# Performance work log

Hardware: AMD Instinct MI355X
Metric: run time of the kernel (lower is better)

## Reference

```python
import jax, jax.numpy as jnp
from jax import lax
import numpy as np

T, B, I, H = 512, 64, 512, 512


def setup_inputs() -> dict:
    key = jax.random.key(0)
    k0, k1, k2, k3, k4 = jax.random.split(key, 5)
    s = 1.0 / np.sqrt(H)  # PyTorch LSTM init range
    x = jax.random.normal(k0, (T, B, I), dtype=jnp.float32)
    W_ih = jax.random.uniform(k1, (4 * H, I), jnp.float32, -s, s)
    W_hh = jax.random.uniform(k2, (4 * H, H), jnp.float32, -s, s)
    b_ih = jax.random.uniform(k3, (4 * H,), jnp.float32, -s, s)
    b_hh = jax.random.uniform(k4, (4 * H,), jnp.float32, -s, s)
    return {"x": x, "W_ih": W_ih, "W_hh": W_hh, "b_ih": b_ih, "b_hh": b_hh}


def reference(x, W_ih, W_hh, b_ih, b_hh):
    # x: [T, B, I] (seq-first, like nn.LSTM with batch_first=False)
    Bv = x.shape[1]
    Hv = W_hh.shape[1]
    # Precompute input projections for all timesteps: [T, B, 4H]
    x_proj = jnp.einsum('tbi,gi->tbg', x, W_ih) + b_ih + b_hh

    def step(carry, xp):
        h, c = carry
        gates = xp + h @ W_hh.T  # [B, 4H]
        i, f, g, o = jnp.split(gates, 4, axis=-1)  # PyTorch gate order i,f,g,o
        i = jax.nn.sigmoid(i)
        f = jax.nn.sigmoid(f)
        g = jnp.tanh(g)
        o = jax.nn.sigmoid(o)
        c = f * c + i * g
        h = o * jnp.tanh(c)
        return (h, c), h

    h0 = jnp.zeros((Bv, Hv), dtype=x.dtype)
    c0 = jnp.zeros((Bv, Hv), dtype=x.dtype)
    _, ys = lax.scan(step, (h0, c0), x_proj)
    return ys  # [T, B, H]
```

## Files before the change

### kernel.cpp

```cpp
#include <hip/hip_runtime.h>


#define T_STEPS 512
#define BATCH   64
#define HID     512
#define NB      64
#define CNT_STRIDE 16

typedef short bf16x8 __attribute__((ext_vector_type(8)));
typedef float f32x4  __attribute__((ext_vector_type(4)));

struct U16B { unsigned long long x, y; };

__device__ __forceinline__ unsigned short f2bf(float f) {
    unsigned int u = __builtin_bit_cast(unsigned int, f);
    u += 0x7FFFu + ((u >> 16) & 1u);
    return (unsigned short)(u >> 16);
}
__device__ __forceinline__ unsigned int pack2(float lo, float hi) {
    return (unsigned int)f2bf(lo) | ((unsigned int)f2bf(hi) << 16);
}
__device__ __forceinline__ uint4 cvt8(const float* __restrict__ p) {
    float4 f0 = *(const float4*)p;
    float4 f1 = *(const float4*)(p + 4);
    uint4 r;
    r.x = pack2(f0.x, f0.y);
    r.y = pack2(f0.z, f0.w);
    r.z = pack2(f1.x, f1.y);
    r.w = pack2(f1.z, f1.w);
    return r;
}
__device__ __forceinline__ void store_cg16(void* p, uint4 v) {
    unsigned long long* q = (unsigned long long*)p;
    U16B u = __builtin_bit_cast(U16B, v);
    __hip_atomic_store(q,     u.x, __ATOMIC_RELAXED, __HIP_MEMORY_SCOPE_AGENT);
    __hip_atomic_store(q + 1, u.y, __ATOMIC_RELAXED, __HIP_MEMORY_SCOPE_AGENT);
}
__device__ __forceinline__ float sigmoidf_(float x) {
    return 1.0f / (1.0f + __expf(-x));
}
__device__ __forceinline__ float tanhf_(float x) {
    x = fminf(fmaxf(x, -15.f), 15.f);
    float e = __expf(2.0f * x);
    return (e - 1.0f) / (e + 1.0f);
}

extern "C" __global__ void __launch_bounds__(256, 1)
lstm_fused(const float* __restrict__ x,
           const float* __restrict__ W_ih,
           const float* __restrict__ W_hh,
           const float* __restrict__ b_ih,
           const float* __restrict__ b_hh,
           float* __restrict__ out,
           unsigned int* __restrict__ cnt,
           unsigned short* __restrict__ hbuf)
{
    __shared__ uint4 sB[2][2][16][64];
    __shared__ __align__(16) unsigned short sH[4][16][8];
    __shared__ __align__(16) float          sHf[4][16][8];

    const int blk  = blockIdx.x;
    const int tid  = threadIdx.x;
    const int w    = tid >> 6;
    const int lane = tid & 63;
    const int l15  = lane & 15;
    const int quad = lane >> 4;
    const int hc0  = blk * 8;

    for (int u = tid; u < 2 * 16 * 64; u += 256) {
        int nt   = u >> 10;
        int kk   = (u >> 6) & 15;
        int ln   = u & 63;
        int c    = (ln & 15) + (nt << 4);
        int grow = ((c >> 3) << 9) + hc0 + (c & 7);
        int k0   = kk * 32 + ((ln >> 4) << 3);
        sB[0][nt][kk][ln] = cvt8(W_ih + grow * 512 + k0);
        sB[1][nt][kk][ln] = cvt8(W_hh + grow * 512 + k0);
    }

    float bias0, bias1;
    {
        int c0 = l15,      g0 = ((c0 >> 3) << 9) + hc0 + (c0 & 7);
        int c1 = l15 + 16, g1 = ((c1 >> 3) << 9) + hc0 + (c1 & 7);
        bias0 = b_ih[g0] + b_hh[g0];
        bias1 = b_ih[g1] + b_hh[g1];
    }
    __syncthreads();

    float cst[4] = {0.f, 0.f, 0.f, 0.f};
    const int aoff = (((w << 4) + l15) * 512) + (quad << 3);
    char* const hb_base = (char*)hbuf;
    const int   hread_off = (quad << 10) + (((w << 4) + l15) << 4);
    long long budget = 300000LL;

    for (int t = 0; t < T_STEPS; ++t) {
        f32x4 acc0 = {0.f, 0.f, 0.f, 0.f};
        f32x4 acc1 = {0.f, 0.f, 0.f, 0.f};

        const float* xt = x + (size_t)t * (BATCH * 512) + aoff;
#pragma unroll
        for (int kk = 0; kk < 16; ++kk) {
            bf16x8 a  = __builtin_bit_cast(bf16x8, cvt8(xt + kk * 32));
            bf16x8 b0 = __builtin_bit_cast(bf16x8, sB[0][0][kk][lane]);
            bf16x8 b1 = __builtin_bit_cast(bf16x8, sB[0][1][kk][lane]);
            acc0 = __builtin_amdgcn_mfma_f32_16x16x32_bf16(a, b0, acc0, 0, 0, 0);
            acc1 = __builtin_amdgcn_mfma_f32_16x16x32_bf16(a, b1, acc1, 0, 0, 0);
        }

        if (t > 0) {
            if (tid == 0) {
                const unsigned int* cp = cnt + (size_t)(t - 1) * CNT_STRIDE;
                while (budget > 0) {
                    unsigned int v = __hip_atomic_load(cp, __ATOMIC_RELAXED,
                                                       __HIP_MEMORY_SCOPE_AGENT);
                    if (v >= NB) break;
                    __builtin_amdgcn_s_sleep(1);
                    --budget;
                }
            }
            __syncthreads();

            const char* hp = hb_base + (((t - 1) & 1) << 16) + hread_off;
            U16B ha[16];
#pragma unroll
            for (int kk = 0; kk < 16; ++kk) {
                const unsigned long long* q =
                    (const unsigned long long*)(hp + (kk << 12));
                ha[kk].x = __hip_atomic_load(q,     __ATOMIC_RELAXED,
                                             __HIP_MEMORY_SCOPE_AGENT);
                ha[kk].y = __hip_atomic_load(q + 1, __ATOMIC_RELAXED,
                                             __HIP_MEMORY_SCOPE_AGENT);
            }
#pragma unroll
            for (int kk = 0; kk < 16; ++kk) {
                bf16x8 a  = __builtin_bit_cast(bf16x8, ha[kk]);
                bf16x8 b0 = __builtin_bit_cast(bf16x8, sB[1][0][kk][lane]);
                bf16x8 b1 = __builtin_bit_cast(bf16x8, sB[1][1][kk][lane]);
                acc0 = __builtin_amdgcn_mfma_f32_16x16x32_bf16(a, b0, acc0, 0, 0, 0);
                acc1 = __builtin_amdgcn_mfma_f32_16x16x32_bf16(a, b1, acc1, 0, 0, 0);
            }
        }

        float gi[4], gf[4], gg[4], go[4];
#pragma unroll
        for (int r = 0; r < 4; ++r) {
            float a0 = acc0[r] + bias0;
            float a1 = acc1[r] + bias1;
            float p0 = __shfl_xor(a0, 8, 64);
            float p1 = __shfl_xor(a1, 8, 64);
            gi[r] = a0; gg[r] = a1; gf[r] = p0; go[r] = p1;
        }
        if (l15 < 8) {
#pragma unroll
            for (int r = 0; r < 4; ++r) {
                float iv = sigmoidf_(gi[r]);
                float fv = sigmoidf_(gf[r]);
                float gv = tanhf_(gg[r]);
                float ov = sigmoidf_(go[r]);
                cst[r] = fv * cst[r] + iv * gv;
                float hv = ov * tanhf_(cst[r]);
                sH [w][(quad << 2) + r][l15] = f2bf(hv);
                sHf[w][(quad << 2) + r][l15] = hv;
            }
        }
        asm volatile("s_waitcnt lgkmcnt(0)" ::: "memory");
        if (lane < 16) {
            uint4 v = *(const uint4*)&sH[w][lane][0];
            char* dst = hb_base + ((t & 1) << 16) + (blk << 10)
                        + (((w << 4) + lane) << 4);
            store_cg16(dst, v);
        }
        asm volatile("s_waitcnt vmcnt(0)" ::: "memory");
        __syncthreads();
        if (tid == 0) {
            (void)__hip_atomic_fetch_add(cnt + (size_t)t * CNT_STRIDE, 1u,
                                         __ATOMIC_RELAXED, __HIP_MEMORY_SCOPE_AGENT);
        }

        if (lane < 32) {
            int row  = lane & 15;
            int half = lane >> 4;
            uint4 v = *(const uint4*)&sHf[w][row][half << 2];
            float* op = out + (size_t)t * (BATCH * HID)
                        + (size_t)((w << 4) + row) * HID + hc0 + (half << 2);
            *(uint4*)op = v;
        }
    }
}

extern "C" void kernel_launch(void* const* d_in, const int* in_sizes, int n_in,
                              void* d_out, int out_size, void* d_ws, size_t ws_size,
                              hipStream_t stream) {
    const float* x    = (const float*)d_in[0];
    const float* W_ih = (const float*)d_in[1];
    const float* W_hh = (const float*)d_in[2];
    const float* b_ih = (const float*)d_in[3];
    const float* b_hh = (const float*)d_in[4];
    float* out = (float*)d_out;

    unsigned int*   cnt = (unsigned int*)d_ws;
    const size_t    cnt_bytes = (size_t)T_STEPS * CNT_STRIDE * sizeof(unsigned int);
    unsigned short* hbuf = (unsigned short*)((char*)d_ws + cnt_bytes);

    (void)hipMemsetAsync(cnt, 0, cnt_bytes, stream);

    hipLaunchKernelGGL(lstm_fused, dim3(NB), dim3(256), 0, stream,
                       x, W_ih, W_hh, b_ih, b_hh, out, cnt, hbuf);
}
```

Before: 3.948 ms.

## Replace global step counter barrier with per-wave flag polling across blocks

Result: slower. 4.030 ms (+2.1%).

```diff
diff --git a/kernel.cpp b/kernel.cpp
--- a/kernel.cpp
+++ b/kernel.cpp
@@ -5,7 +5,6 @@
 #define BATCH   64
 #define HID     512
 #define NB      64
-#define CNT_STRIDE 16
 
 typedef short bf16x8 __attribute__((ext_vector_type(8)));
 typedef float f32x4  __attribute__((ext_vector_type(4)));
@@ -52,7 +51,7 @@
            const float* __restrict__ b_ih,
            const float* __restrict__ b_hh,
            float* __restrict__ out,
-           unsigned int* __restrict__ cnt,
+           unsigned int* __restrict__ flags,
            unsigned short* __restrict__ hbuf)
 {
     __shared__ uint4 sB[2][2][16][64];
@@ -91,9 +90,17 @@
     const int aoff = (((w << 4) + l15) * 512) + (quad << 3);
     char* const hb_base = (char*)hbuf;
     const int   hread_off = (quad << 10) + (((w << 4) + l15) << 4);
-    long long budget = 300000LL;
+    unsigned int* const       my_flag = flags + (w << 6) + blk;
+    const unsigned int* const poll_p  = flags + (w << 6) + lane;
+    long long budget = 400000LL;
 
     for (int t = 0; t < T_STEPS; ++t) {
+        unsigned int early = 0u;
+        if (t > 0)
+            early = __hip_atomic_load(poll_p, __ATOMIC_RELAXED,
+                                      __HIP_MEMORY_SCOPE_AGENT);
+        __builtin_amdgcn_sched_barrier(0);
+
         f32x4 acc0 = {0.f, 0.f, 0.f, 0.f};
         f32x4 acc1 = {0.f, 0.f, 0.f, 0.f};
 
@@ -108,17 +115,15 @@
         }
 
         if (t > 0) {
-            if (tid == 0) {
-                const unsigned int* cp = cnt + (size_t)(t - 1) * CNT_STRIDE;
+            const unsigned int tgt = (unsigned int)t;
+            if (!__all(early >= tgt)) {
                 while (budget > 0) {
-                    unsigned int v = __hip_atomic_load(cp, __ATOMIC_RELAXED,
+                    unsigned int v = __hip_atomic_load(poll_p, __ATOMIC_RELAXED,
                                                        __HIP_MEMORY_SCOPE_AGENT);
-                    if (v >= NB) break;
-                    __builtin_amdgcn_s_sleep(1);
+                    if (__all(v >= tgt)) break;
                     --budget;
                 }
             }
-            __syncthreads();
 
             const char* hp = hb_base + (((t - 1) & 1) << 16) + hread_off;
             U16B ha[16];
@@ -171,10 +176,9 @@
             store_cg16(dst, v);
         }
         asm volatile("s_waitcnt vmcnt(0)" ::: "memory");
-        __syncthreads();
-        if (tid == 0) {
-            (void)__hip_atomic_fetch_add(cnt + (size_t)t * CNT_STRIDE, 1u,
-                                         __ATOMIC_RELAXED, __HIP_MEMORY_SCOPE_AGENT);
+        if (lane == 0) {
+            __hip_atomic_store(my_flag, (unsigned int)(t + 1),
+                               __ATOMIC_RELAXED, __HIP_MEMORY_SCOPE_AGENT);
         }
 
         if (lane < 32) {
@@ -198,12 +202,12 @@
     const float* b_hh = (const float*)d_in[4];
     float* out = (float*)d_out;
 
-    unsigned int*   cnt = (unsigned int*)d_ws;
-    const size_t    cnt_bytes = (size_t)T_STEPS * CNT_STRIDE * sizeof(unsigned int);
-    unsigned short* hbuf = (unsigned short*)((char*)d_ws + cnt_bytes);
-
-    (void)hipMemsetAsync(cnt, 0, cnt_bytes, stream);
+    unsigned int*   flags = (unsigned int*)d_ws;
+    const size_t    flag_bytes = 4 * NB * sizeof(unsigned int);
+    unsigned short* hbuf = (unsigned short*)((char*)d_ws + 1024);
+
+    (void)hipMemsetAsync(flags, 0, flag_bytes, stream);
 
     hipLaunchKernelGGL(lstm_fused, dim3(NB), dim3(256), 0, stream,
-                       x, W_ih, W_hh, b_ih, b_hh, out, cnt, hbuf);
-}
+                       x, W_ih, W_hh, b_ih, b_hh, out, flags, hbuf);
+}
```

## Replace counter barrier with per-element step tags in hidden-state buffer

Applied to the files above, without the earlier changes.

New measurement: 4.037 ms. 1.02x slower.

```diff
diff --git a/kernel.cpp b/kernel.cpp
--- a/kernel.cpp
+++ b/kernel.cpp
@@ -5,7 +5,6 @@
 #define BATCH   64
 #define HID     512
 #define NB      64
-#define CNT_STRIDE 16
 
 typedef short bf16x8 __attribute__((ext_vector_type(8)));
 typedef float f32x4  __attribute__((ext_vector_type(4)));
@@ -52,12 +51,11 @@
            const float* __restrict__ b_ih,
            const float* __restrict__ b_hh,
            float* __restrict__ out,
-           unsigned int* __restrict__ cnt,
-           unsigned short* __restrict__ hbuf)
+           unsigned int* __restrict__ hbuf)
 {
     __shared__ uint4 sB[2][2][16][64];
-    __shared__ __align__(16) unsigned short sH[4][16][8];
-    __shared__ __align__(16) float          sHf[4][16][8];
+    __shared__ __align__(16) unsigned int sHt[4][16][8];
+    __shared__ __align__(16) float        sHf[4][16][8];
 
     const int blk  = blockIdx.x;
     const int tid  = threadIdx.x;
@@ -89,9 +87,9 @@
 
     float cst[4] = {0.f, 0.f, 0.f, 0.f};
     const int aoff = (((w << 4) + l15) * 512) + (quad << 3);
-    char* const hb_base = (char*)hbuf;
-    const int   hread_off = (quad << 10) + (((w << 4) + l15) << 4);
-    long long budget = 300000LL;
+    char* const hb_base  = (char*)hbuf;
+    const int   hread_off = (quad << 11) + (((w << 4) + l15) << 5);
+    long long budget = 2000000LL;
 
     for (int t = 0; t < T_STEPS; ++t) {
         f32x4 acc0 = {0.f, 0.f, 0.f, 0.f};
@@ -108,32 +106,42 @@
         }
 
         if (t > 0) {
-            if (tid == 0) {
-                const unsigned int* cp = cnt + (size_t)(t - 1) * CNT_STRIDE;
-                while (budget > 0) {
-                    unsigned int v = __hip_atomic_load(cp, __ATOMIC_RELAXED,
-                                                       __HIP_MEMORY_SCOPE_AGENT);
-                    if (v >= NB) break;
-                    __builtin_amdgcn_s_sleep(1);
-                    --budget;
+            const char* hp = hb_base + (((t - 1) & 1) << 17) + hread_off;
+            const unsigned int tgt = (unsigned int)t;
+            unsigned long long hw[64];
+            for (;;) {
+#pragma unroll
+                for (int kk = 0; kk < 16; ++kk) {
+                    const unsigned long long* q =
+                        (const unsigned long long*)(hp + (kk << 13));
+#pragma unroll
+                    for (int j = 0; j < 4; ++j)
+                        hw[kk * 4 + j] = __hip_atomic_load(q + j, __ATOMIC_RELAXED,
+                                                           __HIP_MEMORY_SCOPE_AGENT);
                 }
+                unsigned int m = 0;
+#pragma unroll
+                for (int i = 0; i < 64; ++i)
+                    m |= ((unsigned int)hw[i] ^ tgt) & 0xffffu;
+                if (__all(m == 0)) break;
+                if (--budget < 0) break;
             }
-            __syncthreads();
-
-            const char* hp = hb_base + (((t - 1) & 1) << 16) + hread_off;
-            U16B ha[16];
 #pragma unroll
             for (int kk = 0; kk < 16; ++kk) {
-                const unsigned long long* q =
-                    (const unsigned long long*)(hp + (kk << 12));
-                ha[kk].x = __hip_atomic_load(q,     __ATOMIC_RELAXED,
-                                             __HIP_MEMORY_SCOPE_AGENT);
-                ha[kk].y = __hip_atomic_load(q + 1, __ATOMIC_RELAXED,
-                                             __HIP_MEMORY_SCOPE_AGENT);
-            }
-#pragma unroll
-            for (int kk = 0; kk < 16; ++kk) {
-                bf16x8 a  = __builtin_bit_cast(bf16x8, ha[kk]);
+                unsigned int w0 = (unsigned int)(hw[4 * kk + 0]);
+                unsigned int w1 = (unsigned int)(hw[4 * kk + 0] >> 32);
+                unsigned int w2 = (unsigned int)(hw[4 * kk + 1]);
+                unsigned int w3 = (unsigned int)(hw[4 * kk + 1] >> 32);
+                unsigned int w4 = (unsigned int)(hw[4 * kk + 2]);
+                unsigned int w5 = (unsigned int)(hw[4 * kk + 2] >> 32);
+                unsigned int w6 = (unsigned int)(hw[4 * kk + 3]);
+                unsigned int w7 = (unsigned int)(hw[4 * kk + 3] >> 32);
+                uint4 u;
+                u.x = (w0 >> 16) | (w1 & 0xffff0000u);
+                u.y = (w2 >> 16) | (w3 & 0xffff0000u);
+                u.z = (w4 >> 16) | (w5 & 0xffff0000u);
+                u.w = (w6 >> 16) | (w7 & 0xffff0000u);
+                bf16x8 a  = __builtin_bit_cast(bf16x8, u);
                 bf16x8 b0 = __builtin_bit_cast(bf16x8, sB[1][0][kk][lane]);
                 bf16x8 b1 = __builtin_bit_cast(bf16x8, sB[1][1][kk][lane]);
                 acc0 = __builtin_amdgcn_mfma_f32_16x16x32_bf16(a, b0, acc0, 0, 0, 0);
@@ -150,6 +158,7 @@
             float p1 = __shfl_xor(a1, 8, 64);
             gi[r] = a0; gg[r] = a1; gf[r] = p0; go[r] = p1;
         }
+        const unsigned int tagv = (unsigned int)(t + 1);
         if (l15 < 8) {
 #pragma unroll
             for (int r = 0; r < 4; ++r) {
@@ -159,22 +168,19 @@
                 float ov = sigmoidf_(go[r]);
                 cst[r] = fv * cst[r] + iv * gv;
                 float hv = ov * tanhf_(cst[r]);
-                sH [w][(quad << 2) + r][l15] = f2bf(hv);
+                sHt[w][(quad << 2) + r][l15] =
+                    ((unsigned int)f2bf(hv) << 16) | tagv;
                 sHf[w][(quad << 2) + r][l15] = hv;
             }
         }
         asm volatile("s_waitcnt lgkmcnt(0)" ::: "memory");
-        if (lane < 16) {
-            uint4 v = *(const uint4*)&sH[w][lane][0];
-            char* dst = hb_base + ((t & 1) << 16) + (blk << 10)
-                        + (((w << 4) + lane) << 4);
+        if (lane < 32) {
+            int row  = lane >> 1;
+            int half = lane & 1;
+            uint4 v = *(const uint4*)&sHt[w][row][half << 2];
+            char* dst = hb_base + ((t & 1) << 17) + (blk << 11)
+                        + (((w << 4) + row) << 5) + (half << 4);
             store_cg16(dst, v);
-        }
-        asm volatile("s_waitcnt vmcnt(0)" ::: "memory");
-        __syncthreads();
-        if (tid == 0) {
-            (void)__hip_atomic_fetch_add(cnt + (size_t)t * CNT_STRIDE, 1u,
-                                         __ATOMIC_RELAXED, __HIP_MEMORY_SCOPE_AGENT);
         }
 
         if (lane < 32) {
@@ -198,12 +204,9 @@
     const float* b_hh = (const float*)d_in[4];
     float* out = (float*)d_out;
 
-    unsigned int*   cnt = (unsigned int*)d_ws;
-    const size_t    cnt_bytes = (size_t)T_STEPS * CNT_STRIDE * sizeof(unsigned int);
-    unsigned short* hbuf = (unsigned short*)((char*)d_ws + cnt_bytes);
-
-    (void)hipMemsetAsync(cnt, 0, cnt_bytes, stream);
+    unsigned int* hbuf = (unsigned int*)d_ws;
+    (void)hipMemsetAsync(hbuf, 0, 2 * NB * 64 * 8 * sizeof(unsigned int), stream);
 
     hipLaunchKernelGGL(lstm_fused, dim3(NB), dim3(256), 0, stream,
-                       x, W_ih, W_hh, b_ih, b_hh, out, cnt, hbuf);
-}
+                       x, W_ih, W_hh, b_ih, b_hh, out, hbuf);
+}
```
